# Performance work log

Hardware: AMD Instinct MI355X
Metric: run time of the kernel (lower is better)

The kernel has to match this reference:

```python
import jax, jax.numpy as jnp
import numpy as np

N, E, L, H, C, F, NCLASS, NGRAPH = 50000, 800000, 3, 2, 64, 128, 10, 64
NEG_SLOPE = 0.2


def setup_inputs() -> dict:
    key = jax.random.key(0)
    ks = jax.random.split(key, 8)
    x = jax.random.normal(ks[0], (N, F), dtype=jnp.float32)
    edge_index = jax.random.randint(ks[1], (2, E), 0, N, dtype=jnp.int64)
    batch = jnp.sort(jax.random.randint(ks[2], (N,), 0, NGRAPH, dtype=jnp.int64))
    s = 1.0 / np.sqrt(F)
    W = jax.random.normal(ks[3], (L, F, H * C), dtype=jnp.float32) * s
    att_src = jax.random.normal(ks[4], (L, H, C), dtype=jnp.float32) * s
    att_dst = jax.random.normal(ks[5], (L, H, C), dtype=jnp.float32) * s
    bias = jnp.zeros((L, H * C), dtype=jnp.float32)
    lin_w = jax.random.normal(ks[6], (H * C, NCLASS), dtype=jnp.float32) * s
    lin_b = jnp.zeros((NCLASS,), dtype=jnp.float32)
    return {"x": x, "edge_index": edge_index, "batch": batch, "W": W,
            "att_src": att_src, "att_dst": att_dst, "bias": bias,
            "lin_w": lin_w, "lin_b": lin_b}


def _gat_layer(x, src, dst, w, a_s, a_d, b):
    n = x.shape[0]
    h = (x @ w).reshape(n, H, C)                      # [N,H,C]
    alpha_src = jnp.sum(h * a_s, axis=-1)             # [N,H]
    alpha_dst = jnp.sum(h * a_d, axis=-1)             # [N,H]
    e = jax.nn.leaky_relu(alpha_src[src] + alpha_dst[dst], NEG_SLOPE)  # [E2,H]
    # scatter-softmax over incoming edges of each destination node
    m = jax.ops.segment_max(e, dst, num_segments=n)
    p = jnp.exp(e - m[dst])
    z = jax.ops.segment_sum(p, dst, num_segments=n)
    alpha = p / z[dst]                                # [E2,H]
    msg = h[src] * alpha[:, :, None]                  # [E2,H,C]
    out = jax.ops.segment_sum(msg, dst, num_segments=n)  # [N,H,C]
    return out.reshape(n, H * C) + b


def reference(x, edge_index, batch, W, att_src, att_dst, bias, lin_w, lin_b):
    n = x.shape[0]
    # PyG GATConv default: add self-loops
    loop = jnp.arange(n, dtype=edge_index.dtype)
    src = jnp.concatenate([edge_index[0], loop])
    dst = jnp.concatenate([edge_index[1], loop])
    for l in range(L):
        x = _gat_layer(x, src, dst, W[l], att_src[l], att_dst[l], bias[l])
        x = jax.nn.elu(x)  # activation; dropout/bn inactive (eval, use_bn=False)
    # global mean pool per graph
    sums = jax.ops.segment_sum(x, batch, num_segments=NGRAPH)
    cnt = jax.ops.segment_sum(jnp.ones((n,), x.dtype), batch, num_segments=NGRAPH)
    pooled = sums / jnp.maximum(cnt, 1.0)[:, None]    # [NGRAPH, H*C]
    logits = pooled @ lin_w + lin_b
    return jax.nn.softmax(logits, axis=1)
```

## Files before the change

### kernel.cpp

```cpp
#include <hip/hip_runtime.h>
#include <math.h>

#define NNODES 50000
#define NEDGES 800000
#define NLAYERS 3
#define NHEADS 2
#define NCH 64
#define FDIM 128
#define NCLS 10
#define NGRAPH 64
#define NEG_SLOPE 0.2f
#define GEMMB ((NNODES + 63) / 64)
#define NB 391
#define RADB 391
#define PCH 8

#define WAVE_SYNC()                      \
  do {                                   \
    __builtin_amdgcn_wave_barrier();     \
    __asm__ volatile("" ::: "memory");   \
  } while (0)

typedef __attribute__((ext_vector_type(8))) short bf16x8;
typedef __attribute__((ext_vector_type(4))) float f32x4;
typedef __attribute__((ext_vector_type(2))) float f32x2;

__device__ __forceinline__ unsigned short f2bf(float f) {
  unsigned int u = __builtin_bit_cast(unsigned int, f);
  unsigned int r = u + 0x7FFFu + ((u >> 16) & 1u);
  return (unsigned short)(r >> 16);
}
__device__ __forceinline__ float bflo(unsigned v) {
  return __builtin_bit_cast(float, v << 16);
}
__device__ __forceinline__ float bfhi(unsigned v) {
  return __builtin_bit_cast(float, v & 0xFFFF0000u);
}

__global__ __launch_bounds__(256) void k_wprep(const float* __restrict__ W,
                                               unsigned* __restrict__ Wt) {
  __shared__ float Lt[128][132];
  int l = blockIdx.x;
  const float* Wl = W + (size_t)l * FDIM * FDIM;
  unsigned* Wtl = Wt + (size_t)l * FDIM * FDIM / 2;
  int t = threadIdx.x;
#pragma unroll
  for (int i = 0; i < 16; ++i) {
    int k = (t >> 5) + 8 * i;
    int n4 = (t & 31) * 4;
    float4 v = *(const float4*)(Wl + (size_t)k * 128 + n4);
    Lt[k][n4 + 0] = v.x;
    Lt[k][n4 + 1] = v.y;
    Lt[k][n4 + 2] = v.z;
    Lt[k][n4 + 3] = v.w;
  }
  __syncthreads();
  int n = t >> 1;
  int kh = (t & 1) * 64;
  for (int kk = 0; kk < 64; kk += 2) {
    unsigned pk = (unsigned)f2bf(Lt[kh + kk][n]) |
                  ((unsigned)f2bf(Lt[kh + kk + 1][n]) << 16);
    Wtl[n * 64 + (kh >> 1) + (kk >> 1)] = pk;
  }
}

__global__ __launch_bounds__(128) void k_goff(const int* __restrict__ batch,
                                              int* __restrict__ goff,
                                              float* __restrict__ gsum,
                                              int* __restrict__ bcnt) {
  int t = threadIdx.x;
  if (t < NGRAPH) {
    int lo = 0, hi = NNODES;
    while (lo < hi) {
      int mid = (lo + hi) >> 1;
      if (batch[mid] < t) lo = mid + 1;
      else hi = mid;
    }
    goff[t] = lo;
  }
  if (t == 0) goff[NGRAPH] = NNODES;
  for (int i = t; i < NGRAPH * FDIM; i += 128) gsum[i] = 0.f;
  for (int i = t; i < NB; i += 128) bcnt[i] = 0;
}

__device__ __forceinline__ void gemm_body(int blk, const float* __restrict__ X,
                                          const unsigned* __restrict__ Wt,
                                          const float* __restrict__ a_sL,
                                          const float* __restrict__ a_dL,
                                          unsigned* __restrict__ Hb,
                                          float* __restrict__ as_,
                                          float* __restrict__ ad_) {
  int t = threadIdx.x;
  int lane = t & 63;
  int w = t >> 6;
  int row0 = blk * 64;
  int n16 = lane & 15;
  int quad = lane >> 4;
  int m0 = w * 16;

  int gr = row0 + m0 + n16;
  const float* xp = X + (size_t)min(gr, NNODES - 1) * 128;

  f32x4 acc[8];
#pragma unroll
  for (int nt = 0; nt < 8; ++nt) {
    f32x4 z = {0.f, 0.f, 0.f, 0.f};
    acc[nt] = z;
  }
#pragma unroll
  for (int kk = 0; kk < 4; ++kk) {
    float4 va = *(const float4*)(xp + kk * 32 + quad * 8);
    float4 vb = *(const float4*)(xp + kk * 32 + quad * 8 + 4);
    bf16x8 af;
    af[0] = (short)f2bf(va.x); af[1] = (short)f2bf(va.y);
    af[2] = (short)f2bf(va.z); af[3] = (short)f2bf(va.w);
    af[4] = (short)f2bf(vb.x); af[5] = (short)f2bf(vb.y);
    af[6] = (short)f2bf(vb.z); af[7] = (short)f2bf(vb.w);
#pragma unroll
    for (int nt = 0; nt < 8; ++nt) {
      bf16x8 bf = *(const bf16x8*)(Wt + (size_t)(nt * 16 + n16) * 64 +
                                   kk * 16 + quad * 4);
      acc[nt] =
          __builtin_amdgcn_mfma_f32_16x16x32_bf16(af, bf, acc[nt], 0, 0, 0);
    }
  }

  float asv[8], adv[8];
#pragma unroll
  for (int nt = 0; nt < 8; ++nt) {
    asv[nt] = a_sL[nt * 16 + n16];
    adv[nt] = a_dL[nt * 16 + n16];
  }
#pragma unroll
  for (int r = 0; r < 4; ++r) {
    int row = row0 + m0 + quad * 4 + r;
    bool ok = (row < NNODES);
    float ps0 = 0.f, pd0 = 0.f, ps1 = 0.f, pd1 = 0.f;
#pragma unroll
    for (int nt = 0; nt < 4; ++nt) {
      ps0 += acc[nt][r] * asv[nt];
      pd0 += acc[nt][r] * adv[nt];
      ps1 += acc[nt + 4][r] * asv[nt + 4];
      pd1 += acc[nt + 4][r] * adv[nt + 4];
    }
#pragma unroll
    for (int off = 1; off < 16; off <<= 1) {
      ps0 += __shfl_xor(ps0, off, 64);
      pd0 += __shfl_xor(pd0, off, 64);
      ps1 += __shfl_xor(ps1, off, 64);
      pd1 += __shfl_xor(pd1, off, 64);
    }
    if (ok && n16 == 0) {
      as_[row * 2 + 0] = ps0;
      as_[row * 2 + 1] = ps1;
      ad_[row * 2 + 0] = pd0;
      ad_[row * 2 + 1] = pd1;
    }
    if (ok) {
#pragma unroll
      for (int nt = 0; nt < 4; ++nt) {
        unsigned pk = (unsigned)f2bf(acc[nt][r]) |
                      ((unsigned)f2bf(acc[nt + 4][r]) << 16);
        Hb[(size_t)row * 64 + nt * 16 + n16] = pk;
      }
    }
  }
}

__global__ __launch_bounds__(256) void k_gemm(const float* __restrict__ X,
                                              const unsigned* __restrict__ Wt,
                                              const float* __restrict__ a_sL,
                                              const float* __restrict__ a_dL,
                                              unsigned* __restrict__ Hb,
                                              float* __restrict__ as_,
                                              float* __restrict__ ad_) {
  gemm_body(blockIdx.x, X, Wt, a_sL, a_dL, Hb, as_, ad_);
}

__global__ __launch_bounds__(256) void k_front(
    const float* __restrict__ X, const unsigned* __restrict__ Wt,
    const float* __restrict__ a_sL, const float* __restrict__ a_dL,
    unsigned* __restrict__ Hb, float* __restrict__ as_,
    float* __restrict__ ad_, const int* __restrict__ ei, int* __restrict__ bh,
    int* __restrict__ bcnt) {
  int b = blockIdx.x;
  if (b < GEMMB) {
    gemm_body(b, X, Wt, a_sL, a_dL, Hb, as_, ad_);
  } else {
    __shared__ int hist[NB];
    int blk = b - GEMMB;
    int t = threadIdx.x;
    for (int i = t; i < NB; i += 256) hist[i] = 0;
    __syncthreads();
    int e0 = blk * 2048;
#pragma unroll
    for (int i = 0; i < 8; ++i) {
      int e = e0 + i * 256 + t;
      if (e < NEDGES) atomicAdd(&hist[ei[NEDGES + e] >> 7], 1);
    }
    __syncthreads();
    for (int i = t; i < NB; i += 256) {
      int c = hist[i];
      int base = c ? atomicAdd(&bcnt[i], c) : 0;
      bh[i * RADB + blk] = base;
    }
  }
}

__global__ __launch_bounds__(256) void k_bscan(const int* __restrict__ bcnt,
                                               int* __restrict__ bstart) {
  __shared__ int ps[256];
  int t = threadIdx.x;
  int x0 = (2 * t < NB) ? bcnt[2 * t] : 0;
  int x1 = (2 * t + 1 < NB) ? bcnt[2 * t + 1] : 0;
  int pair = x0 + x1;
  ps[t] = pair;
  __syncthreads();
  for (int off = 1; off < 256; off <<= 1) {
    int v = (t >= off) ? ps[t - off] : 0;
    __syncthreads();
    ps[t] += v;
    __syncthreads();
  }
  int ex = ps[t] - pair;
  if (2 * t < NB) bstart[2 * t] = ex;
  if (2 * t + 1 < NB) bstart[2 * t + 1] = ex + x0;
  if (t == 0) bstart[NB] = NEDGES;
}

__global__ __launch_bounds__(256) void k_passB(const int* __restrict__ ei,
                                               const int* __restrict__ bstart,
                                               const int* __restrict__ bh,
                                               unsigned* __restrict__ ebuf) {
  __shared__ int curs[NB];
  int blk = blockIdx.x, t = threadIdx.x;
  for (int i = t; i < NB; i += 256) curs[i] = bstart[i] + bh[i * RADB + blk];
  __syncthreads();
  int e0 = blk * 2048;
#pragma unroll
  for (int i = 0; i < 8; ++i) {
    int e = e0 + i * 256 + t;
    if (e < NEDGES) {
      int s = ei[e];
      int d = ei[NEDGES + e];
      int pos = atomicAdd(&curs[d >> 7], 1);
      ebuf[pos] = ((unsigned)s << 7) | (unsigned)(d & 127);
    }
  }
}

__global__ __launch_bounds__(256) void k_passC(const unsigned* __restrict__ ebuf,
                                               const int* __restrict__ bstart,
                                               int* __restrict__ row_ptr,
                                               int* __restrict__ csr) {
  __shared__ int deg[128];
  __shared__ int scn[128];
  int b = blockIdx.x, t = threadIdx.x;
  int node0 = b * 128;
  int nn = min(128, NNODES - node0);
  int estart = bstart[b];
  int eend = bstart[b + 1];
  if (t < 128) deg[t] = 0;
  __syncthreads();
  for (int e = estart + t; e < eend; e += 256)
    atomicAdd(&deg[ebuf[e] & 127], 1);
  __syncthreads();
  if (t < 128) scn[t] = (t < nn) ? deg[t] + 1 : 0;
  __syncthreads();
  for (int off = 1; off < 128; off <<= 1) {
    int v = (t < 128 && t >= off) ? scn[t - off] : 0;
    __syncthreads();
    if (t < 128) scn[t] += v;
    __syncthreads();
  }
  int base = estart + node0;
  if (t < nn) {
    int st = base + (t ? scn[t - 1] : 0);
    row_ptr[node0 + t] = st;
    csr[st] = node0 + t;
    deg[t] = st + 1;
  }
  if (b == 0 && t == 0) row_ptr[NNODES] = NEDGES + NNODES;
  __syncthreads();
  for (int e = estart + t; e < eend; e += 256) {
    unsigned v = ebuf[e];
    int pos = atomicAdd(&deg[v & 127], 1);
    csr[pos] = (int)(v >> 7);
  }
}

__global__ __launch_bounds__(256) void k_aggregate(
    const unsigned* __restrict__ Hb, const float* __restrict__ as_,
    const float* __restrict__ ad_, const int* __restrict__ row_ptr,
    const int* __restrict__ csr, const float* __restrict__ bias,
    float* __restrict__ Xout) {
  __shared__ f32x2 wb[4][64];
  __shared__ int sb[4][64];
  int wv = threadIdx.x >> 6;
  int lane = threadIdx.x & 63;
  int node = blockIdx.x * 4 + wv;
  if (node >= NNODES) return;
  int rs = row_ptr[node], re = row_ptr[node + 1];
  float2 adv = *(const float2*)&ad_[node * 2];
  const unsigned* Hl = Hb + lane;

  float z0 = 0.f, z1 = 0.f;
  f32x2 A0 = {0.f, 0.f}, A1 = {0.f, 0.f}, A2 = {0.f, 0.f}, A3 = {0.f, 0.f};
  for (int base = rs; base < re; base += 64) {
    int j = base + lane;
    float p0 = 0.f, p1 = 0.f;
    int s = 0;
    if (j < re) {
      s = csr[j];
      float2 asv = *(const float2*)&as_[s * 2];
      float e0 = asv.x + adv.x; e0 = (e0 > 0.f) ? e0 : NEG_SLOPE * e0;
      float e1 = asv.y + adv.y; e1 = (e1 > 0.f) ? e1 : NEG_SLOPE * e1;
      p0 = __expf(e0);
      p1 = __expf(e1);
    }
    z0 += p0;
    z1 += p1;
    f32x2 pp = {p0, p1};
    wb[wv][lane] = pp;
    sb[wv][lane] = s;
    WAVE_SYNC();
    int cl = min(64, re - base);
    int jj = 0;
    for (; jj + 8 <= cl; jj += 8) {
      unsigned v0 = Hl[(size_t)sb[wv][jj + 0] * 64];
      unsigned v1 = Hl[(size_t)sb[wv][jj + 1] * 64];
      unsigned v2 = Hl[(size_t)sb[wv][jj + 2] * 64];
      unsigned v3 = Hl[(size_t)sb[wv][jj + 3] * 64];
      unsigned v4 = Hl[(size_t)sb[wv][jj + 4] * 64];
      unsigned v5 = Hl[(size_t)sb[wv][jj + 5] * 64];
      unsigned v6 = Hl[(size_t)sb[wv][jj + 6] * 64];
      unsigned v7 = Hl[(size_t)sb[wv][jj + 7] * 64];
      f32x2 w0 = wb[wv][jj + 0], w1 = wb[wv][jj + 1];
      f32x2 w2 = wb[wv][jj + 2], w3 = wb[wv][jj + 3];
      f32x2 w4 = wb[wv][jj + 4], w5 = wb[wv][jj + 5];
      f32x2 w6 = wb[wv][jj + 6], w7 = wb[wv][jj + 7];
      f32x2 h0 = {bflo(v0), bfhi(v0)};
      f32x2 h1 = {bflo(v1), bfhi(v1)};
      f32x2 h2 = {bflo(v2), bfhi(v2)};
      f32x2 h3 = {bflo(v3), bfhi(v3)};
      f32x2 h4 = {bflo(v4), bfhi(v4)};
      f32x2 h5 = {bflo(v5), bfhi(v5)};
      f32x2 h6 = {bflo(v6), bfhi(v6)};
      f32x2 h7 = {bflo(v7), bfhi(v7)};
      A0 = h0 * w0 + A0;
      A1 = h1 * w1 + A1;
      A2 = h2 * w2 + A2;
      A3 = h3 * w3 + A3;
      A0 = h4 * w4 + A0;
      A1 = h5 * w5 + A1;
      A2 = h6 * w6 + A2;
      A3 = h7 * w7 + A3;
    }
    for (; jj < cl; ++jj) {
      unsigned v = Hl[(size_t)sb[wv][jj] * 64];
      f32x2 w = wb[wv][jj];
      f32x2 h = {bflo(v), bfhi(v)};
      A0 = h * w + A0;
    }
    WAVE_SYNC();
  }
  f32x2 A = (A0 + A1) + (A2 + A3);
#pragma unroll
  for (int off = 32; off > 0; off >>= 1) {
    z0 += __shfl_xor(z0, off, 64);
    z1 += __shfl_xor(z1, off, 64);
  }
  float o0 = A.x / z0 + bias[lane];
  float o1 = A.y / z1 + bias[64 + lane];
  o0 = (o0 > 0.f) ? o0 : expm1f(o0);
  o1 = (o1 > 0.f) ? o1 : expm1f(o1);
  Xout[(size_t)node * 128 + lane] = o0;
  Xout[(size_t)node * 128 + 64 + lane] = o1;
}

__global__ __launch_bounds__(256) void k_pool2(const float* __restrict__ Xf,
                                               const int* __restrict__ goff,
                                               float* __restrict__ gsum) {
  __shared__ float red[128];
  int b = blockIdx.x;
  int g = b >> 3, ch = b & 7;
  int t = threadIdx.x;
  int c = t & 127, rh = t >> 7;
  int s = goff[g], e = goff[g + 1];
  int len = e - s;
  int c0 = s + (len * ch) / PCH;
  int c1 = s + (len * (ch + 1)) / PCH;
  float acc = 0.f;
  for (int n = c0 + rh; n < c1; n += 2) acc += Xf[(size_t)n * 128 + c];
  if (rh) red[c] = acc;
  __syncthreads();
  if (!rh) atomicAdd(&gsum[g * FDIM + c], acc + red[c]);
}

__global__ __launch_bounds__(64) void k_final(const float* __restrict__ gsum,
                                              const int* __restrict__ goff,
                                              const float* __restrict__ lw,
                                              const float* __restrict__ lb,
                                              float* __restrict__ out) {
  int g = threadIdx.x;
  float cnt = (float)(goff[g + 1] - goff[g]);
  float inv = 1.f / fmaxf(cnt, 1.f);
  float lg[NCLS];
#pragma unroll
  for (int k = 0; k < NCLS; ++k) lg[k] = lb[k];
  for (int c = 0; c < FDIM; ++c) {
    float pv = gsum[g * FDIM + c] * inv;
#pragma unroll
    for (int k = 0; k < NCLS; ++k) lg[k] += pv * lw[c * NCLS + k];
  }
  float mx = lg[0];
#pragma unroll
  for (int k = 1; k < NCLS; ++k) mx = fmaxf(mx, lg[k]);
  float s = 0.f;
#pragma unroll
  for (int k = 0; k < NCLS; ++k) {
    lg[k] = expf(lg[k] - mx);
    s += lg[k];
  }
  float invs = 1.f / s;
#pragma unroll
  for (int k = 0; k < NCLS; ++k) out[g * NCLS + k] = lg[k] * invs;
}


extern "C" void kernel_launch(void* const* d_in, const int* in_sizes, int n_in,
                              void* d_out, int out_size, void* d_ws,
                              size_t ws_size, hipStream_t stream) {
  const float* x = (const float*)d_in[0];
  const int* ei = (const int*)d_in[1];
  const int* batch = (const int*)d_in[2];
  const float* W = (const float*)d_in[3];
  const float* a_s = (const float*)d_in[4];
  const float* a_d = (const float*)d_in[5];
  const float* bias = (const float*)d_in[6];
  const float* lw = (const float*)d_in[7];
  const float* lb = (const float*)d_in[8];
  float* out = (float*)d_out;

  unsigned* Hb = (unsigned*)d_ws;
  float* xb = (float*)(Hb + (size_t)NNODES * 64);
  float* as_ = xb + (size_t)NNODES * 128;
  float* ad_ = as_ + (size_t)NNODES * 2;
  float* gsum = ad_ + (size_t)NNODES * 2;
  int* goff = (int*)(gsum + NGRAPH * FDIM);
  int* bcnt = goff + (NGRAPH + 1);
  int* bstart = bcnt + NB;
  int* row_ptr = bstart + (NB + 1);
  int* csr = row_ptr + (NNODES + 1);
  int* bh = csr + (NEDGES + NNODES);
  unsigned* ebuf = (unsigned*)(bh + NB * RADB);
  unsigned* Wt = ebuf + (NEDGES + 1024);

  k_wprep<<<NLAYERS, 256, 0, stream>>>(W, Wt);
  k_goff<<<1, 128, 0, stream>>>(batch, goff, gsum, bcnt);
  k_front<<<GEMMB + RADB, 256, 0, stream>>>(x, Wt, a_s, a_d, Hb, as_, ad_, ei,
                                            bh, bcnt);
  k_bscan<<<1, 256, 0, stream>>>(bcnt, bstart);
  k_passB<<<RADB, 256, 0, stream>>>(ei, bstart, bh, ebuf);
  k_passC<<<NB, 256, 0, stream>>>(ebuf, bstart, row_ptr, csr);

  for (int l = 0; l < NLAYERS; ++l) {
    if (l > 0) {
      k_gemm<<<GEMMB, 256, 0, stream>>>(xb, Wt + (size_t)l * FDIM * FDIM / 2,
                                        a_s + l * FDIM, a_d + l * FDIM, Hb,
                                        as_, ad_);
    }
    k_aggregate<<<(NNODES + 3) / 4, 256, 0, stream>>>(
        Hb, as_, ad_, row_ptr, csr, bias + l * FDIM, xb);
  }
  k_pool2<<<NGRAPH * PCH, 256, 0, stream>>>(xb, goff, gsum);
  k_final<<<1, 64, 0, stream>>>(gsum, goff, lw, lb, out);
}
```

Before: 334.4 us.

## Split aggregation into softmax and column-quarter gather with quartered H layout

Hb is now stored as four column-quarter planes (16 words per node each). Aggregation is split into a softmax kernel that writes per-edge weights and inverse normalisers, and a gather kernel launched over four quarters, where each wave processes 4 edges at once with 16 lanes per edge. The aim is to shrink each plane's working set so it fits in cache better, and to raise edge-level parallelism for nodes with few neighbours. In exchange, per-edge weights make an extra round trip through global memory and csr is read five times per layer. The k_goff kernel is also folded into k_wprep to save one launch.

```diff
diff --git a/kernel.cpp b/kernel.cpp
--- a/kernel.cpp
+++ b/kernel.cpp
@@ -14,16 +14,11 @@
 #define NB 391
 #define RADB 391
 #define PCH 8
-
-#define WAVE_SYNC()                      \
-  do {                                   \
-    __builtin_amdgcn_wave_barrier();     \
-    __asm__ volatile("" ::: "memory");   \
-  } while (0)
+#define AGG4 (NNODES / 4)
+#define QSZ ((size_t)NNODES * 16)
 
 typedef __attribute__((ext_vector_type(8))) short bf16x8;
 typedef __attribute__((ext_vector_type(4))) float f32x4;
-typedef __attribute__((ext_vector_type(2))) float f32x2;
 
 __device__ __forceinline__ unsigned short f2bf(float f) {
   unsigned int u = __builtin_bit_cast(unsigned int, f);
@@ -38,12 +33,31 @@
 }
 
 __global__ __launch_bounds__(256) void k_wprep(const float* __restrict__ W,
-                                               unsigned* __restrict__ Wt) {
+                                               unsigned* __restrict__ Wt,
+                                               const int* __restrict__ batch,
+                                               int* __restrict__ goff,
+                                               float* __restrict__ gsum,
+                                               int* __restrict__ bcnt) {
   __shared__ float Lt[128][132];
   int l = blockIdx.x;
+  int t = threadIdx.x;
+  if (l == NLAYERS) {
+    if (t < NGRAPH) {
+      int lo = 0, hi = NNODES;
+      while (lo < hi) {
+        int mid = (lo + hi) >> 1;
+        if (batch[mid] < t) lo = mid + 1;
+        else hi = mid;
+      }
+      goff[t] = lo;
+    }
+    if (t == 0) goff[NGRAPH] = NNODES;
+    for (int i = t; i < NGRAPH * FDIM; i += 256) gsum[i] = 0.f;
+    for (int i = t; i < NB; i += 256) bcnt[i] = 0;
+    return;
+  }
   const float* Wl = W + (size_t)l * FDIM * FDIM;
   unsigned* Wtl = Wt + (size_t)l * FDIM * FDIM / 2;
-  int t = threadIdx.x;
 #pragma unroll
   for (int i = 0; i < 16; ++i) {
     int k = (t >> 5) + 8 * i;
@@ -62,25 +76,6 @@
                   ((unsigned)f2bf(Lt[kh + kk + 1][n]) << 16);
     Wtl[n * 64 + (kh >> 1) + (kk >> 1)] = pk;
   }
-}
-
-__global__ __launch_bounds__(128) void k_goff(const int* __restrict__ batch,
-                                              int* __restrict__ goff,
-                                              float* __restrict__ gsum,
-                                              int* __restrict__ bcnt) {
-  int t = threadIdx.x;
-  if (t < NGRAPH) {
-    int lo = 0, hi = NNODES;
-    while (lo < hi) {
-      int mid = (lo + hi) >> 1;
-      if (batch[mid] < t) lo = mid + 1;
-      else hi = mid;
-    }
-    goff[t] = lo;
-  }
-  if (t == 0) goff[NGRAPH] = NNODES;
-  for (int i = t; i < NGRAPH * FDIM; i += 128) gsum[i] = 0.f;
-  for (int i = t; i < NB; i += 128) bcnt[i] = 0;
 }
 
 __device__ __forceinline__ void gemm_body(int blk, const float* __restrict__ X,
@@ -161,7 +156,7 @@
       for (int nt = 0; nt < 4; ++nt) {
         unsigned pk = (unsigned)f2bf(acc[nt][r]) |
                       ((unsigned)f2bf(acc[nt + 4][r]) << 16);
-        Hb[(size_t)row * 64 + nt * 16 + n16] = pk;
+        Hb[(size_t)nt * QSZ + (size_t)row * 16 + n16] = pk;
       }
     }
   }
@@ -289,93 +284,83 @@
   }
 }
 
-__global__ __launch_bounds__(256) void k_aggregate(
-    const unsigned* __restrict__ Hb, const float* __restrict__ as_,
-    const float* __restrict__ ad_, const int* __restrict__ row_ptr,
-    const int* __restrict__ csr, const float* __restrict__ bias,
-    float* __restrict__ Xout) {
-  __shared__ f32x2 wb[4][64];
-  __shared__ int sb[4][64];
+__global__ __launch_bounds__(256) void k_softmax(
+    const float* __restrict__ as_, const float* __restrict__ ad_,
+    const int* __restrict__ row_ptr, const int* __restrict__ csr,
+    float2* __restrict__ pe, float2* __restrict__ zinv) {
   int wv = threadIdx.x >> 6;
   int lane = threadIdx.x & 63;
   int node = blockIdx.x * 4 + wv;
   if (node >= NNODES) return;
   int rs = row_ptr[node], re = row_ptr[node + 1];
   float2 adv = *(const float2*)&ad_[node * 2];
-  const unsigned* Hl = Hb + lane;
-
   float z0 = 0.f, z1 = 0.f;
-  f32x2 A0 = {0.f, 0.f}, A1 = {0.f, 0.f}, A2 = {0.f, 0.f}, A3 = {0.f, 0.f};
-  for (int base = rs; base < re; base += 64) {
-    int j = base + lane;
-    float p0 = 0.f, p1 = 0.f;
-    int s = 0;
-    if (j < re) {
-      s = csr[j];
-      float2 asv = *(const float2*)&as_[s * 2];
-      float e0 = asv.x + adv.x; e0 = (e0 > 0.f) ? e0 : NEG_SLOPE * e0;
-      float e1 = asv.y + adv.y; e1 = (e1 > 0.f) ? e1 : NEG_SLOPE * e1;
-      p0 = __expf(e0);
-      p1 = __expf(e1);
-    }
+  for (int j = rs + lane; j < re; j += 64) {
+    int s = csr[j];
+    float2 asv = *(const float2*)&as_[s * 2];
+    float e0 = asv.x + adv.x; e0 = (e0 > 0.f) ? e0 : NEG_SLOPE * e0;
+    float e1 = asv.y + adv.y; e1 = (e1 > 0.f) ? e1 : NEG_SLOPE * e1;
+    float p0 = __expf(e0);
+    float p1 = __expf(e1);
     z0 += p0;
     z1 += p1;
-    f32x2 pp = {p0, p1};
-    wb[wv][lane] = pp;
-    sb[wv][lane] = s;
-    WAVE_SYNC();
-    int cl = min(64, re - base);
-    int jj = 0;
-    for (; jj + 8 <= cl; jj += 8) {
-      unsigned v0 = Hl[(size_t)sb[wv][jj + 0] * 64];
-      unsigned v1 = Hl[(size_t)sb[wv][jj + 1] * 64];
-      unsigned v2 = Hl[(size_t)sb[wv][jj + 2] * 64];
-      unsigned v3 = Hl[(size_t)sb[wv][jj + 3] * 64];
-      unsigned v4 = Hl[(size_t)sb[wv][jj + 4] * 64];
-      unsigned v5 = Hl[(size_t)sb[wv][jj + 5] * 64];
-      unsigned v6 = Hl[(size_t)sb[wv][jj + 6] * 64];
-      unsigned v7 = Hl[(size_t)sb[wv][jj + 7] * 64];
-      f32x2 w0 = wb[wv][jj + 0], w1 = wb[wv][jj + 1];
-      f32x2 w2 = wb[wv][jj + 2], w3 = wb[wv][jj + 3];
-      f32x2 w4 = wb[wv][jj + 4], w5 = wb[wv][jj + 5];
-      f32x2 w6 = wb[wv][jj + 6], w7 = wb[wv][jj + 7];
-      f32x2 h0 = {bflo(v0), bfhi(v0)};
-      f32x2 h1 = {bflo(v1), bfhi(v1)};
-      f32x2 h2 = {bflo(v2), bfhi(v2)};
-      f32x2 h3 = {bflo(v3), bfhi(v3)};
-      f32x2 h4 = {bflo(v4), bfhi(v4)};
-      f32x2 h5 = {bflo(v5), bfhi(v5)};
-      f32x2 h6 = {bflo(v6), bfhi(v6)};
-      f32x2 h7 = {bflo(v7), bfhi(v7)};
-      A0 = h0 * w0 + A0;
-      A1 = h1 * w1 + A1;
-      A2 = h2 * w2 + A2;
-      A3 = h3 * w3 + A3;
-      A0 = h4 * w4 + A0;
-      A1 = h5 * w5 + A1;
-      A2 = h6 * w6 + A2;
-      A3 = h7 * w7 + A3;
-    }
-    for (; jj < cl; ++jj) {
-      unsigned v = Hl[(size_t)sb[wv][jj] * 64];
-      f32x2 w = wb[wv][jj];
-      f32x2 h = {bflo(v), bfhi(v)};
-      A0 = h * w + A0;
-    }
-    WAVE_SYNC();
-  }
-  f32x2 A = (A0 + A1) + (A2 + A3);
+    pe[j] = make_float2(p0, p1);
+  }
 #pragma unroll
   for (int off = 32; off > 0; off >>= 1) {
     z0 += __shfl_xor(z0, off, 64);
     z1 += __shfl_xor(z1, off, 64);
   }
-  float o0 = A.x / z0 + bias[lane];
-  float o1 = A.y / z1 + bias[64 + lane];
-  o0 = (o0 > 0.f) ? o0 : expm1f(o0);
-  o1 = (o1 > 0.f) ? o1 : expm1f(o1);
-  Xout[(size_t)node * 128 + lane] = o0;
-  Xout[(size_t)node * 128 + 64 + lane] = o1;
+  if (lane == 0) zinv[node] = make_float2(1.f / z0, 1.f / z1);
+}
+
+__global__ __launch_bounds__(256) void k_gather(
+    const unsigned* __restrict__ Hb, const float2* __restrict__ pe,
+    const float2* __restrict__ zinv, const int* __restrict__ row_ptr,
+    const int* __restrict__ csr, const float* __restrict__ bias,
+    float* __restrict__ Xout) {
+  int q = blockIdx.x / AGG4;
+  int blk = blockIdx.x - q * AGG4;
+  int wv = threadIdx.x >> 6;
+  int lane = threadIdx.x & 63;
+  int node = blk * 4 + wv;
+  int rs = row_ptr[node], re = row_ptr[node + 1];
+  int g = lane >> 4, l = lane & 15;
+  const unsigned* Ht = Hb + (size_t)q * QSZ + l;
+  float ax = 0.f, ay = 0.f;
+  for (int j0 = rs; j0 < re; j0 += 8) {
+    int ja = j0 + g;
+    int jb = j0 + 4 + g;
+    bool va = ja < re, vb = jb < re;
+    int jja = va ? ja : rs;
+    int jjb = vb ? jb : rs;
+    int sa = csr[jja];
+    int sb_ = csr[jjb];
+    float2 pa = pe[jja];
+    float2 pb = pe[jjb];
+    unsigned ha = Ht[(size_t)sa * 16];
+    unsigned hb2 = Ht[(size_t)sb_ * 16];
+    if (!va) { pa.x = 0.f; pa.y = 0.f; }
+    if (!vb) { pb.x = 0.f; pb.y = 0.f; }
+    ax += pa.x * bflo(ha);
+    ay += pa.y * bfhi(ha);
+    ax += pb.x * bflo(hb2);
+    ay += pb.y * bfhi(hb2);
+  }
+  ax += __shfl_xor(ax, 16, 64);
+  ay += __shfl_xor(ay, 16, 64);
+  ax += __shfl_xor(ax, 32, 64);
+  ay += __shfl_xor(ay, 32, 64);
+  if (g == 0) {
+    float2 zi = zinv[node];
+    int c = q * 16 + l;
+    float o0 = ax * zi.x + bias[c];
+    float o1 = ay * zi.y + bias[64 + c];
+    o0 = (o0 > 0.f) ? o0 : expm1f(o0);
+    o1 = (o1 > 0.f) ? o1 : expm1f(o1);
+    Xout[(size_t)node * 128 + c] = o0;
+    Xout[(size_t)node * 128 + 64 + c] = o1;
+  }
 }
 
 __global__ __launch_bounds__(256) void k_pool2(const float* __restrict__ Xf,
@@ -446,7 +431,9 @@
   float* xb = (float*)(Hb + (size_t)NNODES * 64);
   float* as_ = xb + (size_t)NNODES * 128;
   float* ad_ = as_ + (size_t)NNODES * 2;
-  float* gsum = ad_ + (size_t)NNODES * 2;
+  float2* pe = (float2*)(ad_ + (size_t)NNODES * 2);
+  float2* zinv = pe + (NEDGES + NNODES);
+  float* gsum = (float*)(zinv + NNODES);
   int* goff = (int*)(gsum + NGRAPH * FDIM);
   int* bcnt = goff + (NGRAPH + 1);
   int* bstart = bcnt + NB;
@@ -456,8 +443,7 @@
   unsigned* ebuf = (unsigned*)(bh + NB * RADB);
   unsigned* Wt = ebuf + (NEDGES + 1024);
 
-  k_wprep<<<NLAYERS, 256, 0, stream>>>(W, Wt);
-  k_goff<<<1, 128, 0, stream>>>(batch, goff, gsum, bcnt);
+  k_wprep<<<NLAYERS + 1, 256, 0, stream>>>(W, Wt, batch, goff, gsum, bcnt);
   k_front<<<GEMMB + RADB, 256, 0, stream>>>(x, Wt, a_s, a_d, Hb, as_, ad_, ei,
                                             bh, bcnt);
   k_bscan<<<1, 256, 0, stream>>>(bcnt, bstart);
@@ -470,8 +456,9 @@
                                         a_s + l * FDIM, a_d + l * FDIM, Hb,
                                         as_, ad_);
     }
-    k_aggregate<<<(NNODES + 3) / 4, 256, 0, stream>>>(
-        Hb, as_, ad_, row_ptr, csr, bias + l * FDIM, xb);
+    k_softmax<<<AGG4, 256, 0, stream>>>(as_, ad_, row_ptr, csr, pe, zinv);
+    k_gather<<<4 * AGG4, 256, 0, stream>>>(Hb, pe, zinv, row_ptr, csr,
+                                           bias + l * FDIM, xb);
   }
   k_pool2<<<NGRAPH * PCH, 256, 0, stream>>>(xb, goff, gsum);
   k_final<<<1, 64, 0, stream>>>(gsum, goff, lw, lb, out);
```

Result: slower. 514.1 us (+53.8%).
